# Optimization experiments

Measured on AMD Instinct MI355X. Metric: run time of the kernel, lower is better.

## Reference

```python
import jax, jax.numpy as jnp
import numpy as np

EMBED_DIM = 1024
NUM_HEADS = 16
HEAD_DIM = EMBED_DIM // NUM_HEADS


def layer_norm(x, gamma, beta, eps=1e-5):
    mu = jnp.mean(x, axis=-1, keepdims=True)
    var = jnp.var(x, axis=-1, keepdims=True)
    return (x - mu) * jax.lax.rsqrt(var + eps) * gamma + beta


def setup_inputs() -> dict:
    key = jax.random.key(0)
    ks = jax.random.split(key, 8)
    D = EMBED_DIM
    s = 1.0 / np.sqrt(D)
    x = jax.random.normal(ks[0], (2, 2048, D), dtype=jnp.float32)
    Wq = jax.random.uniform(ks[1], (D, D), jnp.float32, -s, s)
    Wk = jax.random.uniform(ks[2], (D, D), jnp.float32, -s, s)
    Wv = jax.random.uniform(ks[3], (D, D), jnp.float32, -s, s)
    W1 = jax.random.uniform(ks[4], (D, 4 * D), jnp.float32, -s, s)
    b1 = jnp.zeros((4 * D,), jnp.float32)
    W2 = jax.random.uniform(ks[5], (4 * D, D), jnp.float32, -1.0 / np.sqrt(4 * D), 1.0 / np.sqrt(4 * D))
    b2 = jnp.zeros((D,), jnp.float32)
    g1 = jnp.ones((D,), jnp.float32); be1 = jnp.zeros((D,), jnp.float32)
    g2 = jnp.ones((D,), jnp.float32); be2 = jnp.zeros((D,), jnp.float32)
    return {"x": x, "Wq": Wq, "Wk": Wk, "Wv": Wv, "W1": W1, "b1": b1,
            "W2": W2, "b2": b2, "g1": g1, "be1": be1, "g2": g2, "be2": be2}


def reference(x, Wq, Wk, Wv, W1, b1, W2, b2, g1, be1, g2, be2):
    B, S, D = x.shape
    H, Hd = NUM_HEADS, HEAD_DIM
    x_norm = layer_norm(x, g1, be1)
    # QKV projections (no bias), split into heads: [B, H, S, Hd]
    q = (x_norm @ Wq).reshape(B, S, H, Hd).transpose(0, 2, 1, 3)
    k = (x_norm @ Wk).reshape(B, S, H, Hd).transpose(0, 2, 1, 3)
    v = (x_norm @ Wv).reshape(B, S, H, Hd).transpose(0, 2, 1, 3)
    energy = jnp.einsum('bhqd,bhkd->bhqk', q, k)
    attn = jax.nn.softmax(energy / jnp.sqrt(jnp.float32(Hd)), axis=-1)
    out = jnp.einsum('bhqk,bhkd->bhqd', attn, v)
    attention = out.transpose(0, 2, 1, 3).reshape(B, S, D)
    x_res = attention + x
    x_norm2 = layer_norm(x_res, g2, be2)
    # Faithful quirk: FFN applied to x_res (not x_norm2)
    ffn_out = jax.nn.relu(x_res @ W1 + b1) @ W2 + b2
    return ffn_out + x_norm2
```

## Files before the change

kernel.cpp:

```cpp
#include <hip/hip_runtime.h>
#include <hip/hip_bf16.h>
#include <stdint.h>

typedef __hip_bfloat16 bf16;
typedef __attribute__((ext_vector_type(4))) float f32x4;
typedef __attribute__((ext_vector_type(8))) short s16x8;
typedef __attribute__((ext_vector_type(4))) short s16x4;

#define DEV static __device__ __forceinline__

DEV short f2bf(float f) {
  bf16 h = __float2bfloat16(f);
  short s;
  __builtin_memcpy(&s, &h, 2);
  return s;
}
DEV float bf2f(short s) {
  bf16 h;
  __builtin_memcpy(&h, &s, 2);
  return __bfloat162float(h);
}

__global__ __launch_bounds__(256) void transpose_cvt(
    const float* __restrict__ W, bf16* __restrict__ Wt, int K, int N)
{
  __shared__ float tile[32][33];
  const int n0 = blockIdx.x << 5;
  const int k0 = blockIdx.y << 5;
  const int tx = threadIdx.x & 31, ty = threadIdx.x >> 5;
#pragma unroll
  for (int i = 0; i < 4; ++i)
    tile[ty + i * 8][tx] = W[(size_t)(k0 + ty + i * 8) * N + n0 + tx];
  __syncthreads();
#pragma unroll
  for (int i = 0; i < 4; ++i)
    Wt[(size_t)(n0 + ty + i * 8) * K + k0 + tx] = __float2bfloat16(tile[tx][ty + i * 8]);
}

__global__ __launch_bounds__(256) void ln_bf16(
    const float* __restrict__ x, const float* __restrict__ g,
    const float* __restrict__ be, bf16* __restrict__ out)
{
  const int t = threadIdx.x;
  const size_t row = blockIdx.x;
  const float4 v = ((const float4*)(x + row * 1024))[t];
  float s = v.x + v.y + v.z + v.w;
  float ss = v.x * v.x + v.y * v.y + v.z * v.z + v.w * v.w;
#pragma unroll
  for (int off = 32; off > 0; off >>= 1) {
    s += __shfl_down(s, off);
    ss += __shfl_down(ss, off);
  }
  __shared__ float sh[8];
  const int wave = t >> 6, lane = t & 63;
  if (!lane) { sh[wave] = s; sh[4 + wave] = ss; }
  __syncthreads();
  s = sh[0] + sh[1] + sh[2] + sh[3];
  ss = sh[4] + sh[5] + sh[6] + sh[7];
  const float mean = s * (1.f / 1024.f);
  const float rstd = rsqrtf(ss * (1.f / 1024.f) - mean * mean + 1e-5f);
  const float4 gv = ((const float4*)g)[t];
  const float4 bv = ((const float4*)be)[t];
  s16x4 o;
  o[0] = f2bf((v.x - mean) * rstd * gv.x + bv.x);
  o[1] = f2bf((v.y - mean) * rstd * gv.y + bv.y);
  o[2] = f2bf((v.z - mean) * rstd * gv.z + bv.z);
  o[3] = f2bf((v.w - mean) * rstd * gv.w + bv.w);
  ((s16x4*)(out + row * 1024))[t] = o;
}

__global__ __launch_bounds__(256) void add_ln_bf16(
    const float* __restrict__ a, const float* __restrict__ x,
    const float* __restrict__ g, const float* __restrict__ be,
    bf16* __restrict__ xres, bf16* __restrict__ xnorm)
{
  const int t = threadIdx.x;
  const size_t row = blockIdx.x;
  const float4 av = ((const float4*)(a + row * 1024))[t];
  const float4 xv = ((const float4*)(x + row * 1024))[t];
  float4 v;
  v.x = av.x + xv.x; v.y = av.y + xv.y; v.z = av.z + xv.z; v.w = av.w + xv.w;
  float s = v.x + v.y + v.z + v.w;
  float ss = v.x * v.x + v.y * v.y + v.z * v.z + v.w * v.w;
#pragma unroll
  for (int off = 32; off > 0; off >>= 1) {
    s += __shfl_down(s, off);
    ss += __shfl_down(ss, off);
  }
  __shared__ float sh[8];
  const int wave = t >> 6, lane = t & 63;
  if (!lane) { sh[wave] = s; sh[4 + wave] = ss; }
  __syncthreads();
  s = sh[0] + sh[1] + sh[2] + sh[3];
  ss = sh[4] + sh[5] + sh[6] + sh[7];
  const float mean = s * (1.f / 1024.f);
  const float rstd = rsqrtf(ss * (1.f / 1024.f) - mean * mean + 1e-5f);
  const float4 gv = ((const float4*)g)[t];
  const float4 bv = ((const float4*)be)[t];
  s16x4 r, o;
  r[0] = f2bf(v.x); r[1] = f2bf(v.y); r[2] = f2bf(v.z); r[3] = f2bf(v.w);
  o[0] = f2bf((v.x - mean) * rstd * gv.x + bv.x);
  o[1] = f2bf((v.y - mean) * rstd * gv.y + bv.y);
  o[2] = f2bf((v.z - mean) * rstd * gv.z + bv.z);
  o[3] = f2bf((v.w - mean) * rstd * gv.w + bv.w);
  ((s16x4*)(xres + row * 1024))[t] = r;
  ((s16x4*)(xnorm + row * 1024))[t] = o;
}

template <int EPI>
__global__ __launch_bounds__(256) void gemm_bt(
    const bf16* __restrict__ A, const bf16* __restrict__ Bt,
    void* __restrict__ C, const float* __restrict__ bias,
    const bf16* __restrict__ add_bf16, int M, int N, int K)
{
  __shared__ bf16 sA0[128 * 64];
  __shared__ bf16 sB0[128 * 64];
  __shared__ bf16 sA1[128 * 64];
  __shared__ bf16 sB1[128 * 64];
  const int tid = threadIdx.x;
  const int wave = tid >> 6, lane = tid & 63;
  const int fr = lane & 15, fg = lane >> 4;
  const int f7 = fr & 7;
  const int wr = wave >> 1, wc = wave & 1;
  const int nbx = N >> 7;
  int bid = blockIdx.x;
  if ((gridDim.x & 7) == 0) {
    const int cpx = gridDim.x >> 3;
    bid = (bid & 7) * cpx + (bid >> 3);
  }
  const int brow = (bid / nbx) << 7;
  const int bcol = (bid % nbx) << 7;

  f32x4 acc[4][4] = {};

  const int rsub = lane >> 3;
  const int cl = (lane & 7) ^ rsub;
  size_t ga[4], gb[4];
  int la[4];
#pragma unroll
  for (int j = 0; j < 4; ++j) {
    const int r = wave * 32 + j * 8;
    ga[j] = (size_t)(brow + r + rsub) * K + cl * 8;
    gb[j] = (size_t)(bcol + r + rsub) * K + cl * 8;
    la[j] = r * 64;
  }

#define GSTAGE(SA, SB, kt)                                                     \
  do {                                                                         \
    _Pragma("unroll")                                                          \
    for (int j = 0; j < 4; ++j) {                                              \
      __builtin_amdgcn_global_load_lds(                                        \
          (const __attribute__((address_space(1))) uint32_t*)(A + ga[j] + (kt)), \
          (__attribute__((address_space(3))) uint32_t*)(&SA[la[j]]), 16, 0, 0);  \
      __builtin_amdgcn_global_load_lds(                                        \
          (const __attribute__((address_space(1))) uint32_t*)(Bt + gb[j] + (kt)),\
          (__attribute__((address_space(3))) uint32_t*)(&SB[la[j]]), 16, 0, 0);  \
    }                                                                          \
  } while (0)

#define COMPUTE(SA, SB)                                                        \
  do {                                                                         \
    s16x8 af[4][2], bfr[4][2];                                                 \
    _Pragma("unroll")                                                          \
    for (int m = 0; m < 4; ++m)                                                \
      _Pragma("unroll")                                                        \
      for (int kk = 0; kk < 2; ++kk)                                           \
        af[m][kk] = *(const s16x8*)(&SA[(wr * 64 + m * 16 + fr) * 64 +         \
                                        (((kk * 4 + fg) ^ f7) << 3)]);         \
    _Pragma("unroll")                                                          \
    for (int n = 0; n < 4; ++n)                                                \
      _Pragma("unroll")                                                        \
      for (int kk = 0; kk < 2; ++kk)                                           \
        bfr[n][kk] = *(const s16x8*)(&SB[(wc * 64 + n * 16 + fr) * 64 +        \
                                         (((kk * 4 + fg) ^ f7) << 3)]);        \
    _Pragma("unroll")                                                          \
    for (int kk = 0; kk < 2; ++kk)                                             \
      _Pragma("unroll")                                                        \
      for (int m = 0; m < 4; ++m)                                              \
        _Pragma("unroll")                                                      \
        for (int n = 0; n < 4; ++n)                                            \
          acc[m][n] = __builtin_amdgcn_mfma_f32_16x16x32_bf16(                 \
              af[m][kk], bfr[n][kk], acc[m][n], 0, 0, 0);                      \
  } while (0)

  GSTAGE(sA0, sB0, 0);
  __syncthreads();

  int kt = 0;
  for (;;) {
    if (kt + 64 < K) {
      GSTAGE(sA1, sB1, kt + 64);
      COMPUTE(sA0, sB0);
      __syncthreads();
    } else {
      COMPUTE(sA0, sB0);
      break;
    }
    kt += 64;
    if (kt + 64 < K) {
      GSTAGE(sA0, sB0, kt + 64);
      COMPUTE(sA1, sB1);
      __syncthreads();
    } else {
      COMPUTE(sA1, sB1);
      break;
    }
    kt += 64;
  }
#undef GSTAGE
#undef COMPUTE

  const int crow = brow + wr * 64;
  const int ccol = bcol + wc * 64;
#pragma unroll
  for (int m = 0; m < 4; ++m) {
#pragma unroll
    for (int n = 0; n < 4; ++n) {
      const int col = ccol + n * 16 + fr;
#pragma unroll
      for (int j = 0; j < 4; ++j) {
        const int row = crow + m * 16 + fg * 4 + j;
        float v = acc[m][n][j];
        if (EPI == 0) {
          ((bf16*)C)[(size_t)row * N + col] = __float2bfloat16(v);
        } else if (EPI == 1) {
          v += bias[col];
          v = fmaxf(v, 0.f);
          ((bf16*)C)[(size_t)row * N + col] = __float2bfloat16(v);
        } else {
          float a;
          {
            bf16 hb = add_bf16[(size_t)row * N + col];
            a = __bfloat162float(hb);
          }
          ((float*)C)[(size_t)row * N + col] = v + bias[col] + a;
        }
      }
    }
  }
}

__global__ __launch_bounds__(512, 4) void attn_fwd(
    const bf16* __restrict__ QK, const bf16* __restrict__ Vt,
    float* __restrict__ Out)
{
  const int LDK = 2048;
  const int qt = blockIdx.x;
  const int bh = blockIdx.y;
  const int b = bh >> 4, h = bh & 15;
  const int tid = threadIdx.x;
  const int wave = tid >> 6, lane = tid & 63;
  const int fr = lane & 15, fg = lane >> 4;
  const int f7 = fr & 7;

  const short* base = (const short*)QK + (size_t)b * 2048 * LDK;
  const short* Qp = base + h * 64;
  const short* Kp = base + 1024 + h * 64;
  const short* Vp = (const short*)Vt + (size_t)h * 64 * 4096 + b * 2048;
  const int q0 = qt * 128 + wave * 16;

  __shared__ short Kbuf[2][64 * 64];
  __shared__ short Vbuf[2][64 * 64];
  __shared__ short P_lds[8][16 * 72];
  short* Pw = P_lds[wave];

  const int rsub = lane >> 3;
  const int clog = (lane & 7) ^ rsub;
  const short* Ksrc = Kp + (size_t)(8 * wave + rsub) * LDK + clog * 8;
  const short* Vsrc = Vp + (size_t)(8 * wave + rsub) * 4096 + clog * 8;

  s16x8 qf0 = *(const s16x8*)(Qp + (size_t)(q0 + fr) * LDK + fg * 8);
  s16x8 qf1 = *(const s16x8*)(Qp + (size_t)(q0 + fr) * LDK + 32 + fg * 8);
#pragma unroll
  for (int i = 0; i < 8; ++i) {
    qf0[i] = f2bf(bf2f(qf0[i]) * 0.125f);
    qf1[i] = f2bf(bf2f(qf1[i]) * 0.125f);
  }

  f32x4 acc[4] = {};
  f32x4 mrow = {-1e30f, -1e30f, -1e30f, -1e30f};
  f32x4 lrow = {};

#define STAGE(bi, kt)                                                          \
  do {                                                                         \
    __builtin_amdgcn_global_load_lds(                                          \
        (const __attribute__((address_space(1))) uint32_t*)(Ksrc + (size_t)(kt) * LDK), \
        (__attribute__((address_space(3))) uint32_t*)(&Kbuf[bi][wave * 512]),  \
        16, 0, 0);                                                             \
    __builtin_amdgcn_global_load_lds(                                          \
        (const __attribute__((address_space(1))) uint32_t*)(Vsrc + (kt)),      \
        (__attribute__((address_space(3))) uint32_t*)(&Vbuf[bi][wave * 512]),  \
        16, 0, 0);                                                             \
  } while (0)

  int cur = 0;
  STAGE(0, 0);

  for (int kt = 0; kt < 2048; kt += 64) {
    if (kt + 64 < 2048) {
      STAGE(cur ^ 1, kt + 64);
      asm volatile("s_waitcnt vmcnt(2)" ::: "memory");
    } else {
      asm volatile("s_waitcnt vmcnt(0)" ::: "memory");
    }
    __builtin_amdgcn_s_barrier();
    __builtin_amdgcn_sched_barrier(0);

    const short* Kb = Kbuf[cur];
    const short* Vb = Vbuf[cur];

    f32x4 e[4];
#pragma unroll
    for (int t = 0; t < 4; ++t) {
      const int ro = (t * 16 + fr) * 64;
      const s16x8 k0 = *(const s16x8*)(Kb + ro + ((fg ^ f7) << 3));
      const s16x8 k1 = *(const s16x8*)(Kb + ro + (((4 + fg) ^ f7) << 3));
      f32x4 z = {};
      z = __builtin_amdgcn_mfma_f32_16x16x32_bf16(qf0, k0, z, 0, 0, 0);
      z = __builtin_amdgcn_mfma_f32_16x16x32_bf16(qf1, k1, z, 0, 0, 0);
      e[t] = z;
    }

    f32x4 lmx;
#pragma unroll
    for (int j = 0; j < 4; ++j)
      lmx[j] = fmaxf(fmaxf(e[0][j], e[1][j]), fmaxf(e[2][j], e[3][j]));
    const bool need = (lmx[0] > mrow[0] + 8.f) | (lmx[1] > mrow[1] + 8.f) |
                      (lmx[2] > mrow[2] + 8.f) | (lmx[3] > mrow[3] + 8.f);
    if (__any(need)) {
      f32x4 mx = lmx;
#pragma unroll
      for (int d = 1; d < 16; d <<= 1)
#pragma unroll
        for (int j = 0; j < 4; ++j) mx[j] = fmaxf(mx[j], __shfl_xor(mx[j], d));
#pragma unroll
      for (int j = 0; j < 4; ++j) {
        const float mn = fmaxf(mrow[j], mx[j]);
        const float al = __expf(mrow[j] - mn);
        lrow[j] *= al;
        mrow[j] = mn;
#pragma unroll
        for (int nn = 0; nn < 4; ++nn) acc[nn][j] *= al;
      }
    }

#pragma unroll
    for (int j = 0; j < 4; ++j) {
#pragma unroll
      for (int t = 0; t < 4; ++t) e[t][j] = __expf(e[t][j] - mrow[j]);
      lrow[j] += (e[0][j] + e[1][j]) + (e[2][j] + e[3][j]);
    }

#pragma unroll
    for (int t = 0; t < 4; ++t)
#pragma unroll
      for (int j = 0; j < 4; ++j)
        Pw[(fg * 4 + j) * 72 + t * 16 + fr] = f2bf(e[t][j]);
    const s16x8 pf0 = *(const s16x8*)(Pw + fr * 72 + fg * 8);
    const s16x8 pf1 = *(const s16x8*)(Pw + fr * 72 + 32 + fg * 8);

#pragma unroll
    for (int nn = 0; nn < 4; ++nn) {
      const int ro = (nn * 16 + fr) * 64;
      const s16x8 vf0 = *(const s16x8*)(Vb + ro + ((fg ^ f7) << 3));
      const s16x8 vf1 = *(const s16x8*)(Vb + ro + (((4 + fg) ^ f7) << 3));
      acc[nn] = __builtin_amdgcn_mfma_f32_16x16x32_bf16(pf0, vf0, acc[nn], 0, 0, 0);
      acc[nn] = __builtin_amdgcn_mfma_f32_16x16x32_bf16(pf1, vf1, acc[nn], 0, 0, 0);
    }

    __builtin_amdgcn_s_barrier();
    __builtin_amdgcn_sched_barrier(0);
    cur ^= 1;
  }
#undef STAGE

#pragma unroll
  for (int d = 1; d < 16; d <<= 1)
#pragma unroll
    for (int j = 0; j < 4; ++j) lrow[j] += __shfl_xor(lrow[j], d);
  f32x4 inv;
#pragma unroll
  for (int j = 0; j < 4; ++j) inv[j] = 1.0f / lrow[j];
  float* outp = Out + (size_t)(b * 2048 + q0) * 1024 + h * 64;
#pragma unroll
  for (int nn = 0; nn < 4; ++nn)
#pragma unroll
    for (int j = 0; j < 4; ++j)
      outp[(size_t)(fg * 4 + j) * 1024 + nn * 16 + fr] = acc[nn][j] * inv[j];
}

extern "C" void kernel_launch(void* const* d_in, const int* in_sizes, int n_in,
                              void* d_out, int out_size, void* d_ws, size_t ws_size,
                              hipStream_t stream)
{
  const float* x   = (const float*)d_in[0];
  const float* Wq  = (const float*)d_in[1];
  const float* Wk  = (const float*)d_in[2];
  const float* Wv  = (const float*)d_in[3];
  const float* W1  = (const float*)d_in[4];
  const float* b1  = (const float*)d_in[5];
  const float* W2  = (const float*)d_in[6];
  const float* b2  = (const float*)d_in[7];
  const float* g1  = (const float*)d_in[8];
  const float* be1 = (const float*)d_in[9];
  const float* g2  = (const float*)d_in[10];
  const float* be2 = (const float*)d_in[11];
  float* out = (float*)d_out;

  const int M = 4096, D = 1024, DF = 4096;

  bf16* Wqk_t = (bf16*)d_ws;
  bf16* Wv_t  = Wqk_t + (size_t)2048 * 1024;
  bf16* W1t   = Wv_t + (size_t)1024 * 1024;
  bf16* W2t   = W1t + (size_t)4096 * 1024;
  bf16* big   = W2t + (size_t)4096 * 1024;
  bf16* QK    = big;
  bf16* Vt    = big + (size_t)8 * 1024 * 1024;
  bf16* hbuf  = big;
  char* p2    = (char*)(big + (size_t)16 * 1024 * 1024);
  bf16* xnorm = (bf16*)p2;
  float* attnO = (float*)p2;
  char* p3    = p2 + (size_t)M * D * sizeof(float);
  bf16* xres  = (bf16*)p3;
  bf16* xnorm2 = xres + (size_t)M * D;

  transpose_cvt<<<dim3(32, 32), 256, 0, stream>>>(Wq, Wqk_t, D, D);
  transpose_cvt<<<dim3(32, 32), 256, 0, stream>>>(Wk, Wqk_t + (size_t)D * D, D, D);
  transpose_cvt<<<dim3(32, 32), 256, 0, stream>>>(Wv, Wv_t, D, D);
  transpose_cvt<<<dim3(128, 32), 256, 0, stream>>>(W1, W1t, D, DF);
  transpose_cvt<<<dim3(32, 128), 256, 0, stream>>>(W2, W2t, DF, D);
  ln_bf16<<<M, 256, 0, stream>>>(x, g1, be1, xnorm);
  gemm_bt<0><<<(M / 128) * (2048 / 128), 256, 0, stream>>>(
      xnorm, Wqk_t, QK, nullptr, nullptr, M, 2048, D);
  gemm_bt<0><<<(D / 128) * (M / 128), 256, 0, stream>>>(
      Wv_t, xnorm, Vt, nullptr, nullptr, D, M, D);
  attn_fwd<<<dim3(16, 32), 512, 0, stream>>>(QK, Vt, attnO);
  add_ln_bf16<<<M, 256, 0, stream>>>(attnO, x, g2, be2, xres, xnorm2);
  gemm_bt<1><<<(M / 128) * (DF / 128), 256, 0, stream>>>(
      xres, W1t, hbuf, b1, nullptr, M, DF, D);
  gemm_bt<2><<<(M / 128) * (D / 128), 256, 0, stream>>>(
      hbuf, W2t, out, b2, xnorm2, M, D, DF);
}
```

Before: 248.0 us.

## Add 512-thread 256x128 triple-buffered GEMM for QK and FFN1, setprio around MFMAs

Adds a new GEMM kernel with 512 threads and 256x128 output tiles, a three-stage LDS ring buffer with prefetch two steps ahead, an XCD-aware block remap, and raised wave priority around the MFMA sections. It replaces the QK projection and FFN first-layer GEMMs, aiming for more operand reuse per block and better hiding of load latency. The attention kernel also gets s_setprio around its MFMA blocks. The cost is much larger LDS use per block (about 144KB) and fewer blocks in the grid, which lowers occupancy.

```diff
diff --git a/kernel.cpp b/kernel.cpp
--- a/kernel.cpp
+++ b/kernel.cpp
@@ -148,13 +148,13 @@
 #define GSTAGE(SA, SB, kt)                                                     \
   do {                                                                         \
     _Pragma("unroll")                                                          \
-    for (int j = 0; j < 4; ++j) {                                              \
+    for (int jj = 0; jj < 4; ++jj) {                                           \
       __builtin_amdgcn_global_load_lds(                                        \
-          (const __attribute__((address_space(1))) uint32_t*)(A + ga[j] + (kt)), \
-          (__attribute__((address_space(3))) uint32_t*)(&SA[la[j]]), 16, 0, 0);  \
+          (const __attribute__((address_space(1))) uint32_t*)(A + ga[jj] + (kt)), \
+          (__attribute__((address_space(3))) uint32_t*)(&SA[la[jj]]), 16, 0, 0);  \
       __builtin_amdgcn_global_load_lds(                                        \
-          (const __attribute__((address_space(1))) uint32_t*)(Bt + gb[j] + (kt)),\
-          (__attribute__((address_space(3))) uint32_t*)(&SB[la[j]]), 16, 0, 0);  \
+          (const __attribute__((address_space(1))) uint32_t*)(Bt + gb[jj] + (kt)),\
+          (__attribute__((address_space(3))) uint32_t*)(&SB[la[jj]]), 16, 0, 0);  \
     }                                                                          \
   } while (0)
 
@@ -240,6 +240,128 @@
   }
 }
 
+template <int EPI>
+__global__ __launch_bounds__(512) void gemm512_bt(
+    const bf16* __restrict__ A, const bf16* __restrict__ Bt,
+    void* __restrict__ C, const float* __restrict__ bias, int M, int N, int K)
+{
+  __shared__ bf16 sA[3][256 * 64];
+  __shared__ bf16 sB[3][128 * 64];
+  const int tid = threadIdx.x;
+  const int wave = tid >> 6, lane = tid & 63;
+  const int fr = lane & 15, fg = lane >> 4;
+  const int f7 = fr & 7;
+  const int wr = wave >> 1, wc = wave & 1;
+  const int nbx = N >> 7;
+  int bid = blockIdx.x;
+  if ((gridDim.x & 7) == 0) {
+    const int cpx = gridDim.x >> 3;
+    bid = (bid & 7) * cpx + (bid >> 3);
+  }
+  const int brow = (bid / nbx) << 8;
+  const int bcol = (bid % nbx) << 7;
+
+  f32x4 acc[4][4] = {};
+
+  const int rsub = lane >> 3;
+  const int cl = (lane & 7) ^ rsub;
+  size_t ga[4], gb[2];
+  int laA[4], laB[2];
+#pragma unroll
+  for (int j = 0; j < 4; ++j) {
+    const int r = j * 64 + wave * 8;
+    ga[j] = (size_t)(brow + r + rsub) * K + cl * 8;
+    laA[j] = r * 64;
+  }
+#pragma unroll
+  for (int j = 0; j < 2; ++j) {
+    const int r = j * 64 + wave * 8;
+    gb[j] = (size_t)(bcol + r + rsub) * K + cl * 8;
+    laB[j] = r * 64;
+  }
+
+#define STG(bi, koff)                                                          \
+  do {                                                                         \
+    _Pragma("unroll")                                                          \
+    for (int jj = 0; jj < 4; ++jj)                                             \
+      __builtin_amdgcn_global_load_lds(                                        \
+          (const __attribute__((address_space(1))) uint32_t*)(A + ga[jj] + (koff)), \
+          (__attribute__((address_space(3))) uint32_t*)(&sA[bi][laA[jj]]), 16, 0, 0); \
+    _Pragma("unroll")                                                          \
+    for (int jj = 0; jj < 2; ++jj)                                             \
+      __builtin_amdgcn_global_load_lds(                                        \
+          (const __attribute__((address_space(1))) uint32_t*)(Bt + gb[jj] + (koff)),\
+          (__attribute__((address_space(3))) uint32_t*)(&sB[bi][laB[jj]]), 16, 0, 0); \
+  } while (0)
+
+  const int nk = K >> 6;
+  STG(0, 0);
+  STG(1, 64);
+
+  int cb = 0;
+  for (int j = 0; j < nk; ++j) {
+    if (j < nk - 1) {
+      asm volatile("s_waitcnt vmcnt(6)" ::: "memory");
+    } else {
+      asm volatile("s_waitcnt vmcnt(0)" ::: "memory");
+    }
+    __builtin_amdgcn_s_barrier();
+    if (j + 2 < nk) {
+      const int tb = (cb + 2) % 3;
+      STG(tb, (j + 2) * 64);
+    }
+    const bf16* SA = sA[cb];
+    const bf16* SB = sB[cb];
+    s16x8 af[4][2], bfr[4][2];
+#pragma unroll
+    for (int m = 0; m < 4; ++m)
+#pragma unroll
+      for (int kk = 0; kk < 2; ++kk)
+        af[m][kk] = *(const s16x8*)(&SA[(wr * 64 + m * 16 + fr) * 64 +
+                                        (((kk * 4 + fg) ^ f7) << 3)]);
+#pragma unroll
+    for (int n = 0; n < 4; ++n)
+#pragma unroll
+      for (int kk = 0; kk < 2; ++kk)
+        bfr[n][kk] = *(const s16x8*)(&SB[(wc * 64 + n * 16 + fr) * 64 +
+                                         (((kk * 4 + fg) ^ f7) << 3)]);
+    __builtin_amdgcn_s_setprio(1);
+#pragma unroll
+    for (int kk = 0; kk < 2; ++kk)
+#pragma unroll
+      for (int m = 0; m < 4; ++m)
+#pragma unroll
+        for (int n = 0; n < 4; ++n)
+          acc[m][n] = __builtin_amdgcn_mfma_f32_16x16x32_bf16(
+              af[m][kk], bfr[n][kk], acc[m][n], 0, 0, 0);
+    __builtin_amdgcn_s_setprio(0);
+    cb = (cb + 1) % 3;
+  }
+#undef STG
+
+  const int crow = brow + wr * 64;
+  const int ccol = bcol + wc * 64;
+#pragma unroll
+  for (int m = 0; m < 4; ++m) {
+#pragma unroll
+    for (int n = 0; n < 4; ++n) {
+      const int col = ccol + n * 16 + fr;
+#pragma unroll
+      for (int j = 0; j < 4; ++j) {
+        const int row = crow + m * 16 + fg * 4 + j;
+        float v = acc[m][n][j];
+        if (EPI == 0) {
+          ((bf16*)C)[(size_t)row * N + col] = __float2bfloat16(v);
+        } else {
+          v += bias[col];
+          v = fmaxf(v, 0.f);
+          ((bf16*)C)[(size_t)row * N + col] = __float2bfloat16(v);
+        }
+      }
+    }
+  }
+}
+
 __global__ __launch_bounds__(512, 4) void attn_fwd(
     const bf16* __restrict__ QK, const bf16* __restrict__ Vt,
     float* __restrict__ Out)
@@ -281,14 +403,14 @@
   f32x4 mrow = {-1e30f, -1e30f, -1e30f, -1e30f};
   f32x4 lrow = {};
 
-#define STAGE(bi, kt)                                                          \
+#define STAGE(bi, koff)                                                        \
   do {                                                                         \
     __builtin_amdgcn_global_load_lds(                                          \
-        (const __attribute__((address_space(1))) uint32_t*)(Ksrc + (size_t)(kt) * LDK), \
+        (const __attribute__((address_space(1))) uint32_t*)(Ksrc + (size_t)(koff) * LDK), \
         (__attribute__((address_space(3))) uint32_t*)(&Kbuf[bi][wave * 512]),  \
         16, 0, 0);                                                             \
     __builtin_amdgcn_global_load_lds(                                          \
-        (const __attribute__((address_space(1))) uint32_t*)(Vsrc + (kt)),      \
+        (const __attribute__((address_space(1))) uint32_t*)(Vsrc + (koff)),    \
         (__attribute__((address_space(3))) uint32_t*)(&Vbuf[bi][wave * 512]),  \
         16, 0, 0);                                                             \
   } while (0)
@@ -310,6 +432,7 @@
     const short* Vb = Vbuf[cur];
 
     f32x4 e[4];
+    __builtin_amdgcn_s_setprio(1);
 #pragma unroll
     for (int t = 0; t < 4; ++t) {
       const int ro = (t * 16 + fr) * 64;
@@ -320,6 +443,7 @@
       z = __builtin_amdgcn_mfma_f32_16x16x32_bf16(qf1, k1, z, 0, 0, 0);
       e[t] = z;
     }
+    __builtin_amdgcn_s_setprio(0);
 
     f32x4 lmx;
 #pragma unroll
@@ -359,6 +483,7 @@
     const s16x8 pf0 = *(const s16x8*)(Pw + fr * 72 + fg * 8);
     const s16x8 pf1 = *(const s16x8*)(Pw + fr * 72 + 32 + fg * 8);
 
+    __builtin_amdgcn_s_setprio(1);
 #pragma unroll
     for (int nn = 0; nn < 4; ++nn) {
       const int ro = (nn * 16 + fr) * 64;
@@ -367,6 +492,7 @@
       acc[nn] = __builtin_amdgcn_mfma_f32_16x16x32_bf16(pf0, vf0, acc[nn], 0, 0, 0);
       acc[nn] = __builtin_amdgcn_mfma_f32_16x16x32_bf16(pf1, vf1, acc[nn], 0, 0, 0);
     }
+    __builtin_amdgcn_s_setprio(0);
 
     __builtin_amdgcn_s_barrier();
     __builtin_amdgcn_sched_barrier(0);
@@ -430,14 +556,14 @@
   transpose_cvt<<<dim3(128, 32), 256, 0, stream>>>(W1, W1t, D, DF);
   transpose_cvt<<<dim3(32, 128), 256, 0, stream>>>(W2, W2t, DF, D);
   ln_bf16<<<M, 256, 0, stream>>>(x, g1, be1, xnorm);
-  gemm_bt<0><<<(M / 128) * (2048 / 128), 256, 0, stream>>>(
-      xnorm, Wqk_t, QK, nullptr, nullptr, M, 2048, D);
+  gemm512_bt<0><<<(M / 256) * (2048 / 128), 512, 0, stream>>>(
+      xnorm, Wqk_t, QK, nullptr, M, 2048, D);
   gemm_bt<0><<<(D / 128) * (M / 128), 256, 0, stream>>>(
       Wv_t, xnorm, Vt, nullptr, nullptr, D, M, D);
   attn_fwd<<<dim3(16, 32), 512, 0, stream>>>(QK, Vt, attnO);
   add_ln_bf16<<<M, 256, 0, stream>>>(attnO, x, g2, be2, xres, xnorm2);
-  gemm_bt<1><<<(M / 128) * (DF / 128), 256, 0, stream>>>(
-      xres, W1t, hbuf, b1, nullptr, M, DF, D);
+  gemm512_bt<1><<<(M / 256) * (DF / 128), 512, 0, stream>>>(
+      xres, W1t, hbuf, b1, M, DF, D);
   gemm_bt<2><<<(M / 128) * (D / 128), 256, 0, stream>>>(
       hbuf, W2t, out, b2, xnorm2, M, D, DF);
 }
```

Measured after the change: 254.7 us. +2.7%, slower.
